# Performance work log

Measured on AMD Instinct MI355X. Metric: run time of the kernel, lower is better.

## Reference

```python
import jax, jax.numpy as jnp
import numpy as np

NEG_BIG = 1e30


def setup_inputs() -> dict:
    key = jax.random.key(0)
    k1, k2, k3, k4 = jax.random.split(key, 4)
    B, S, D, H = 32, 2048, 512, 512
    inp = jax.random.normal(k1, (B, S, D), dtype=jnp.float32)
    state = jax.random.normal(k2, (B, D), dtype=jnp.float32)
    mask = jnp.ones((B, S), dtype=jnp.float32)
    # torch Linear(in=2D, out=H, bias=False) weight is [H, 2D]; store transposed for matmul
    lim1 = np.sqrt(6.0 / (2 * D + H))  # xavier_uniform
    W1 = jax.random.uniform(k3, (2 * D, H), dtype=jnp.float32, minval=-lim1, maxval=lim1)
    lim2 = np.sqrt(6.0 / (H + 1))
    w2 = jax.random.uniform(k4, (H, 1), dtype=jnp.float32, minval=-lim2, maxval=lim2)
    return {"input": inp, "state": state, "mask": mask, "W1": W1, "w2": w2}


def reference(input, state, mask, W1, w2):
    B, S, D = input.shape
    # cat([state_expanded, input], dim=2) @ W1 == state @ W1_top + input @ W1_bot
    W1s, W1x = W1[:D], W1[D:]
    h = jnp.tanh(state @ W1s[:, None, :].squeeze(1)[None] if False else
                 jnp.tanh(jnp.einsum('bd,dh->bh', state, W1s)[:, None, :] +
                          jnp.einsum('bsd,dh->bsh', input, W1x)))
    # (the expression above evaluates the second branch of the dummy conditional)
    att = jnp.einsum('bsh,ho->bso', h, w2)  # [B, S, 1]
    logit = att - NEG_BIG * (1.0 - mask[:, :, None])  # [B, S, 1]
    p = jax.nn.softmax(logit, axis=1)  # [B, S, 1]
    pooled = jnp.sum(input * p, axis=1)  # [B, D]
    return pooled, logit.squeeze(-1)
```

## Files before the change

### kernel.cpp

```cpp
#include <hip/hip_runtime.h>
#include <cstdint>
#include <cstddef>


#define NEG_BIG 1e30f

typedef __attribute__((ext_vector_type(8))) short short8_t;
typedef __attribute__((ext_vector_type(4))) float f32x4;

__device__ inline unsigned short f2bf(float f){
  union { float f; unsigned int u; } v; v.f = f;
  unsigned int r = v.u + 0x7fffu + ((v.u >> 16) & 1u);
  return (unsigned short)(r >> 16);
}
__device__ inline float tanh_cheap(float x){
  return 1.0f - 2.0f*__builtin_amdgcn_rcpf(1.0f + __expf(2.0f*x));
}

typedef __attribute__((address_space(1))) const unsigned int g_u32;
typedef __attribute__((address_space(3))) unsigned int l_u32;
__device__ inline void gload16(const void* g, unsigned short* l){
  __builtin_amdgcn_global_load_lds((g_u32*)g, (l_u32*)l, 16, 0, 0);
}

__global__ __launch_bounds__(256) void k0_prep(const float* __restrict__ state,
                                               const float* __restrict__ W1,
                                               float* __restrict__ sbp,
                                               unsigned short* __restrict__ w1xt){
  const int bid = blockIdx.x, t = threadIdx.x;
  if (bid < 64) {
    const int k0 = (bid >> 3) * 64, h0 = (bid & 7) * 64;
    __shared__ float tile[64][65];
    const int c = t & 63, r0 = t >> 6;
    #pragma unroll
    for (int i = 0; i < 16; ++i){
      int r = r0 + 4*i;
      tile[r][c] = W1[(size_t)(512 + k0 + r)*512 + h0 + c];
    }
    __syncthreads();
    #pragma unroll
    for (int i = 0; i < 16; ++i){
      int r = r0 + 4*i;
      w1xt[(size_t)(h0 + r)*512 + k0 + c] = f2bf(tile[c][r]);
    }
  } else {
    const int idx = bid - 64;
    const int b = idx >> 3, ds = idx & 7;
    __shared__ float stl[64];
    if (t < 64) stl[t] = state[b*512 + ds*64 + t];
    __syncthreads();
    float acc0 = 0.f, acc1 = 0.f;
    #pragma unroll 8
    for (int i = 0; i < 64; ++i){
      const float w = stl[i];
      acc0 += w * W1[(size_t)(ds*64 + i)*512 + t];
      acc1 += w * W1[(size_t)(ds*64 + i)*512 + t + 256];
    }
    sbp[(size_t)(ds*32 + b)*512 + t]       = acc0;
    sbp[(size_t)(ds*32 + b)*512 + t + 256] = acc1;
  }
}

__global__ __launch_bounds__(512, 1) void k1_gemm_f32a(const float* __restrict__ input,
                                                       const unsigned short* __restrict__ w1xt,
                                                       const float* __restrict__ sbp,
                                                       const float* __restrict__ w2,
                                                       float* __restrict__ plog){
  __shared__ unsigned short lds[65536];

  const int orig = blockIdx.x;
  const int xcd = orig & 7, qq = orig >> 3;
  const int mtile = xcd*32 + (qq >> 1);
  const int nt = qq & 1;
  const int m0 = mtile*256, n0 = nt*256;
  const int b = m0 >> 11;

  const int t = threadIdx.x;
  const int lane = t & 63, wid = t >> 6;
  const int wr = wid >> 2, wcn = wid & 3;
  const int lr = lane & 15, kg = lane >> 4;
  const int l7 = lr & 7;

  const int srow = t >> 3;
  const int sinv = (t & 7) ^ ((t >> 3) & 7);
  const float*          gA  = input + (size_t)(m0 + srow)*512 + sinv*4;
  const unsigned short* gBp = w1xt  + (size_t)(n0 + srow)*512 + sinv*8;

  f32x4 acc[8][4];
  #pragma unroll
  for (int mi = 0; mi < 8; ++mi)
    #pragma unroll
    for (int ni = 0; ni < 4; ++ni) acc[mi][ni] = (f32x4){0.f,0.f,0.f,0.f};

  short8_t af[8], bf[2];

#define STAGE_A(KT) do{ \
    const float* gs_ = gA + (KT)*32; \
    const unsigned db_ = (unsigned)((((KT)&1)*16384) + wid*512); \
    gload16(gs_,             &lds[db_]); \
    gload16(gs_ +  64*512,   &lds[db_ + 4096]); \
    gload16(gs_ + 128*512,   &lds[db_ + 8192]); \
    gload16(gs_ + 192*512,   &lds[db_ + 12288]); }while(0)

#define STAGE_B(BT) do{ \
    const unsigned short* gs_ = gBp + (BT)*64; \
    const unsigned db_ = 32768u + (unsigned)((((BT)&1)*16384) + wid*512); \
    gload16(gs_,             &lds[db_]); \
    gload16(gs_ +  64*512,   &lds[db_ + 4096]); \
    gload16(gs_ + 128*512,   &lds[db_ + 8192]); \
    gload16(gs_ + 192*512,   &lds[db_ + 12288]); }while(0)

#define READ_A_ALL(KT) do{ \
    const unsigned ab_ = (unsigned)(((KT)&1)*16384); \
    _Pragma("unroll") for (int mi = 0; mi < 8; ++mi){ \
      const unsigned r_ = (unsigned)(wr*128 + mi*16 + lr); \
      f32x4 lo_ = *(const f32x4*)&lds[ab_ + r_*64 + (unsigned)(((2*kg    ) ^ l7)*8)]; \
      f32x4 hi_ = *(const f32x4*)&lds[ab_ + r_*64 + (unsigned)(((2*kg + 1) ^ l7)*8)]; \
      union { short8_t s; unsigned u[4]; } pk_; \
      asm("v_cvt_pk_bf16_f32 %0, %1, %2" : "=v"(pk_.u[0]) : "v"(lo_[0]), "v"(lo_[1])); \
      asm("v_cvt_pk_bf16_f32 %0, %1, %2" : "=v"(pk_.u[1]) : "v"(lo_[2]), "v"(lo_[3])); \
      asm("v_cvt_pk_bf16_f32 %0, %1, %2" : "=v"(pk_.u[2]) : "v"(hi_[0]), "v"(hi_[1])); \
      asm("v_cvt_pk_bf16_f32 %0, %1, %2" : "=v"(pk_.u[3]) : "v"(hi_[2]), "v"(hi_[3])); \
      af[mi] = pk_.s; \
    } }while(0)

#define READ_B(NH, KT) do{ \
    const unsigned bb_ = 32768u + (unsigned)((((KT)>>1)&1)*16384); \
    const unsigned h4_ = (unsigned)(((KT)&1)*4); \
    _Pragma("unroll") for (int nn = 0; nn < 2; ++nn){ \
      const unsigned rw_ = (unsigned)(wcn*64 + ((NH)*2+nn)*16 + lr); \
      bf[nn] = *(const short8_t*)&lds[bb_ + rw_*64 + (unsigned)(((h4_ + kg) ^ l7)*8)]; } }while(0)

#define MFMA16(NH) do{ \
    __builtin_amdgcn_s_setprio(1); \
    _Pragma("unroll") for (int mi = 0; mi < 8; ++mi) \
      _Pragma("unroll") for (int nn = 0; nn < 2; ++nn) \
        acc[mi][(NH)*2+nn] = __builtin_amdgcn_mfma_f32_16x16x32_bf16(af[mi], bf[nn], acc[mi][(NH)*2+nn], 0,0,0); \
    __builtin_amdgcn_s_setprio(0); }while(0)

  STAGE_A(0); STAGE_B(0); STAGE_A(1);
  asm volatile("s_waitcnt vmcnt(4)" ::: "memory");
  __builtin_amdgcn_s_barrier();

  #pragma unroll
  for (int kt = 0; kt < 16; ++kt){
    READ_A_ALL(kt);
    READ_B(0, kt);
    if ((kt & 1) == 0 && kt + 2 < 16) STAGE_B((kt >> 1) + 1);
    __builtin_amdgcn_s_barrier();
    asm volatile("s_waitcnt lgkmcnt(0)" ::: "memory");
    __builtin_amdgcn_sched_barrier(0);
    MFMA16(0);
    __builtin_amdgcn_s_barrier();
    READ_B(1, kt);
    if (kt + 2 < 16) STAGE_A(kt + 2);
    __builtin_amdgcn_s_barrier();
    asm volatile("s_waitcnt lgkmcnt(0)" ::: "memory");
    __builtin_amdgcn_sched_barrier(0);
    MFMA16(1);
    if (kt < 14){
      if ((kt & 1) == 0) asm volatile("s_waitcnt vmcnt(8)" ::: "memory");
      else               asm volatile("s_waitcnt vmcnt(4)" ::: "memory");
    } else if (kt == 14){
      asm volatile("s_waitcnt vmcnt(0)" ::: "memory");
    }
    __builtin_amdgcn_s_barrier();
  }
#undef STAGE_A
#undef STAGE_B
#undef READ_A_ALL
#undef READ_B
#undef MFMA16

  float w2v[4], sbv[4];
  #pragma unroll
  for (int ni = 0; ni < 4; ++ni){
    const int h = n0 + wcn*64 + ni*16 + lr;
    w2v[ni] = w2[h];
    float s = 0.f;
    #pragma unroll
    for (int ds = 0; ds < 8; ++ds) s += sbp[(size_t)(ds*32 + b)*512 + h];
    sbv[ni] = s;
  }
  float* red = reinterpret_cast<float*>(&lds[0]);
  #pragma unroll
  for (int mi = 0; mi < 8; ++mi){
    #pragma unroll
    for (int j = 0; j < 4; ++j){
      float v = 0.f;
      #pragma unroll
      for (int ni = 0; ni < 4; ++ni)
        v += tanh_cheap(tanh_cheap(acc[mi][ni][j] + sbv[ni])) * w2v[ni];
      v += __shfl_xor(v, 1); v += __shfl_xor(v, 2);
      v += __shfl_xor(v, 4); v += __shfl_xor(v, 8);
      if (lr == 0)
        red[wcn*256 + wr*128 + mi*16 + kg*4 + j] = v;
    }
  }
  __syncthreads();
  if (t < 256)
    plog[(size_t)nt*65536 + m0 + t] = red[t] + red[256+t] + red[512+t] + red[768+t];
}

__global__ __launch_bounds__(256) void k2_softmax(const float* __restrict__ plog,
                                                  const float* __restrict__ mask,
                                                  float* __restrict__ out_logit,
                                                  float* __restrict__ mz){
  const int b = blockIdx.x, t = threadIdx.x;
  float l[8]; float mx = -3.4e38f;
  #pragma unroll
  for (int i = 0; i < 8; ++i){
    const size_t idx = (size_t)b*2048 + t + i*256;
    float v = plog[idx] + plog[65536 + idx];
    v -= NEG_BIG * (1.0f - mask[idx]);
    l[i] = v;
    out_logit[idx] = v;
    mx = fmaxf(mx, v);
  }
  __shared__ float red[8];
  const int wid = t >> 6, lane = t & 63;
  #pragma unroll
  for (int off = 1; off < 64; off <<= 1) mx = fmaxf(mx, __shfl_xor(mx, off));
  if (lane == 0) red[wid] = mx;
  __syncthreads();
  mx = fmaxf(fmaxf(red[0], red[1]), fmaxf(red[2], red[3]));
  float zs = 0.f;
  #pragma unroll
  for (int i = 0; i < 8; ++i) zs += __expf(l[i] - mx);
  #pragma unroll
  for (int off = 1; off < 64; off <<= 1) zs += __shfl_xor(zs, off);
  if (lane == 0) red[4 + wid] = zs;
  __syncthreads();
  if (t == 0){ mz[b*2] = mx; mz[b*2+1] = red[4]+red[5]+red[6]+red[7]; }
}

__global__ __launch_bounds__(256) void k3_pool(const float* __restrict__ input,
                                               const float* __restrict__ logit,
                                               const float* __restrict__ mz,
                                               float* __restrict__ pool){
  const int b = blockIdx.x >> 4, sc = blockIdx.x & 15;
  const int t = threadIdx.x;
  __shared__ float p[128];
  const float m = mz[b*2], invZ = 1.0f / mz[b*2+1];
  if (t < 128) p[t] = __expf(logit[(size_t)b*2048 + sc*128 + t] - m) * invZ;
  __syncthreads();
  const int half = t >> 7, cw = t & 127;
  float a0=0.f,a1=0.f,a2=0.f,a3=0.f;
  const float* base = input + ((size_t)b*2048 + sc*128 + half)*512 + cw*4;
  #pragma unroll 4
  for (int i = 0; i < 64; ++i){
    const float4 v = *reinterpret_cast<const float4*>(base + (size_t)i*1024);
    const float pv = p[half + 2*i];
    a0 += pv*v.x; a1 += pv*v.y; a2 += pv*v.z; a3 += pv*v.w;
  }
  float4 o = {a0,a1,a2,a3};
  *reinterpret_cast<float4*>(pool + (size_t)blockIdx.x*1024 + half*512 + cw*4) = o;
}

__global__ __launch_bounds__(256) void k4_reduce(const float* __restrict__ pool,
                                                 float* __restrict__ out_pooled){
  const int tg = blockIdx.x*256 + threadIdx.x;
  const int b = tg >> 9, d = tg & 511;
  float s = 0.f;
  #pragma unroll
  for (int c = 0; c < 32; ++c) s += pool[((size_t)b*32 + c)*512 + d];
  out_pooled[tg] = s;
}

extern "C" void kernel_launch(void* const* d_in, const int* in_sizes, int n_in,
                              void* d_out, int out_size, void* d_ws, size_t ws_size,
                              hipStream_t stream){
  const float* input = (const float*)d_in[0];
  const float* state = (const float*)d_in[1];
  const float* mask  = (const float*)d_in[2];
  const float* W1    = (const float*)d_in[3];
  const float* w2    = (const float*)d_in[4];

  float* out_pooled = (float*)d_out;
  float* out_logit  = (float*)d_out + 16384;

  char* ws = (char*)d_ws;
  float*          sbp  = (float*)(ws);
  unsigned short* w1xt = (unsigned short*)(ws + 524288);
  float*          plog = (float*)(ws + 1048576);
  float*          mz   = (float*)(ws + 1572864);
  float*          pool = (float*)(ws + 1573120);
  (void)ws_size; (void)in_sizes; (void)n_in; (void)out_size;

  k0_prep     <<<320, 256, 0, stream>>>(state, W1, sbp, w1xt);
  k1_gemm_f32a<<<512, 512, 0, stream>>>(input, w1xt, sbp, w2, plog);
  k2_softmax  <<<32,  256, 0, stream>>>(plog, mask, out_logit, mz);
  k3_pool     <<<512, 256, 0, stream>>>(input, out_logit, mz, pool);
  k4_reduce   <<<64,  256, 0, stream>>>(pool, out_pooled);
}
```

Before: 101.2 us.

## Split MFMA phases by M-half and stage next A tile one iteration ahead

The inner loop now splits each k-step's MFMA work into two M halves instead of two N halves. It loads four A fragments per half and all four B fragments at once, which shrinks the live fragment register set. The A prefetch is issued at the start of each iteration for the next k-tile rather than two ahead mid-iteration. Each iteration ends with a full vmcnt(0) wait instead of the graded partial waits. This may lower register pressure and simplify the schedule, but it shortens how far global loads run ahead of compute, so memory latency may be exposed.

```diff
diff --git a/kernel.cpp b/kernel.cpp
--- a/kernel.cpp
+++ b/kernel.cpp
@@ -19,7 +19,7 @@
 
 typedef __attribute__((address_space(1))) const unsigned int g_u32;
 typedef __attribute__((address_space(3))) unsigned int l_u32;
-__device__ inline void gload16(const void* g, unsigned short* l){
+__device__ inline void gload16(const void* g, void* l){
   __builtin_amdgcn_global_load_lds((g_u32*)g, (l_u32*)l, 16, 0, 0);
 }
 
@@ -92,7 +92,7 @@
     #pragma unroll
     for (int ni = 0; ni < 4; ++ni) acc[mi][ni] = (f32x4){0.f,0.f,0.f,0.f};
 
-  short8_t af[8], bf[2];
+  short8_t af[4], bf[4];
 
 #define STAGE_A(KT) do{ \
     const float* gs_ = gA + (KT)*32; \
@@ -110,10 +110,10 @@
     gload16(gs_ + 128*512,   &lds[db_ + 8192]); \
     gload16(gs_ + 192*512,   &lds[db_ + 12288]); }while(0)
 
-#define READ_A_ALL(KT) do{ \
+#define READ_A_HALF(MH, KT) do{ \
     const unsigned ab_ = (unsigned)(((KT)&1)*16384); \
-    _Pragma("unroll") for (int mi = 0; mi < 8; ++mi){ \
-      const unsigned r_ = (unsigned)(wr*128 + mi*16 + lr); \
+    _Pragma("unroll") for (int mm = 0; mm < 4; ++mm){ \
+      const unsigned r_ = (unsigned)(wr*128 + ((MH)*4+mm)*16 + lr); \
       f32x4 lo_ = *(const f32x4*)&lds[ab_ + r_*64 + (unsigned)(((2*kg    ) ^ l7)*8)]; \
       f32x4 hi_ = *(const f32x4*)&lds[ab_ + r_*64 + (unsigned)(((2*kg + 1) ^ l7)*8)]; \
       union { short8_t s; unsigned u[4]; } pk_; \
@@ -121,21 +121,21 @@
       asm("v_cvt_pk_bf16_f32 %0, %1, %2" : "=v"(pk_.u[1]) : "v"(lo_[2]), "v"(lo_[3])); \
       asm("v_cvt_pk_bf16_f32 %0, %1, %2" : "=v"(pk_.u[2]) : "v"(hi_[0]), "v"(hi_[1])); \
       asm("v_cvt_pk_bf16_f32 %0, %1, %2" : "=v"(pk_.u[3]) : "v"(hi_[2]), "v"(hi_[3])); \
-      af[mi] = pk_.s; \
+      af[mm] = pk_.s; \
     } }while(0)
 
-#define READ_B(NH, KT) do{ \
+#define READ_B_ALL(KT) do{ \
     const unsigned bb_ = 32768u + (unsigned)((((KT)>>1)&1)*16384); \
     const unsigned h4_ = (unsigned)(((KT)&1)*4); \
-    _Pragma("unroll") for (int nn = 0; nn < 2; ++nn){ \
-      const unsigned rw_ = (unsigned)(wcn*64 + ((NH)*2+nn)*16 + lr); \
+    _Pragma("unroll") for (int nn = 0; nn < 4; ++nn){ \
+      const unsigned rw_ = (unsigned)(wcn*64 + nn*16 + lr); \
       bf[nn] = *(const short8_t*)&lds[bb_ + rw_*64 + (unsigned)(((h4_ + kg) ^ l7)*8)]; } }while(0)
 
-#define MFMA16(NH) do{ \
+#define MFMA16(MH) do{ \
     __builtin_amdgcn_s_setprio(1); \
-    _Pragma("unroll") for (int mi = 0; mi < 8; ++mi) \
-      _Pragma("unroll") for (int nn = 0; nn < 2; ++nn) \
-        acc[mi][(NH)*2+nn] = __builtin_amdgcn_mfma_f32_16x16x32_bf16(af[mi], bf[nn], acc[mi][(NH)*2+nn], 0,0,0); \
+    _Pragma("unroll") for (int mm = 0; mm < 4; ++mm) \
+      _Pragma("unroll") for (int nn = 0; nn < 4; ++nn) \
+        acc[(MH)*4+mm][nn] = __builtin_amdgcn_mfma_f32_16x16x32_bf16(af[mm], bf[nn], acc[(MH)*4+mm][nn], 0,0,0); \
     __builtin_amdgcn_s_setprio(0); }while(0)
 
   STAGE_A(0); STAGE_B(0); STAGE_A(1);
@@ -144,32 +144,27 @@
 
   #pragma unroll
   for (int kt = 0; kt < 16; ++kt){
-    READ_A_ALL(kt);
-    READ_B(0, kt);
+    READ_A_HALF(0, kt);
+    READ_B_ALL(kt);
+    if (kt >= 1 && kt + 1 < 16) STAGE_A(kt + 1);
     if ((kt & 1) == 0 && kt + 2 < 16) STAGE_B((kt >> 1) + 1);
     __builtin_amdgcn_s_barrier();
     asm volatile("s_waitcnt lgkmcnt(0)" ::: "memory");
     __builtin_amdgcn_sched_barrier(0);
     MFMA16(0);
     __builtin_amdgcn_s_barrier();
-    READ_B(1, kt);
-    if (kt + 2 < 16) STAGE_A(kt + 2);
+    READ_A_HALF(1, kt);
     __builtin_amdgcn_s_barrier();
     asm volatile("s_waitcnt lgkmcnt(0)" ::: "memory");
     __builtin_amdgcn_sched_barrier(0);
     MFMA16(1);
-    if (kt < 14){
-      if ((kt & 1) == 0) asm volatile("s_waitcnt vmcnt(8)" ::: "memory");
-      else               asm volatile("s_waitcnt vmcnt(4)" ::: "memory");
-    } else if (kt == 14){
-      asm volatile("s_waitcnt vmcnt(0)" ::: "memory");
-    }
+    if (kt < 15) asm volatile("s_waitcnt vmcnt(0)" ::: "memory");
     __builtin_amdgcn_s_barrier();
   }
 #undef STAGE_A
 #undef STAGE_B
-#undef READ_A_ALL
-#undef READ_B
+#undef READ_A_HALF
+#undef READ_B_ALL
 #undef MFMA16
 
   float w2v[4], sbv[4];
```

Measured after the change: 97.22 us. 1.04x faster.
